# Kernel optimization log

Hardware: AMD Instinct MI355X
Metric: run time of the kernel (lower is better)

Reference implementation:

```python
import jax, jax.numpy as jnp
import numpy as np

TD_DENOM = 3600.0  # td_upper - td_lower
SD_DENOM = 1000.0  # sd_upper - sd_lower

B, T, E, H = 64, 256, 512, 512
V, NB = 50000, 128


def setup_inputs() -> dict:
    key = jax.random.key(0)
    ks = jax.random.split(key, 16)
    s = 0.02
    return {
        'loc_seq': jax.random.randint(ks[0], (B, T), 0, V),
        'td_upper_seq': jax.random.randint(ks[1], (B, T), 0, NB),
        'td_lower_seq': jax.random.randint(ks[2], (B, T), 0, NB),
        'sd_upper_seq': jax.random.randint(ks[3], (B, T), 0, NB),
        'sd_lower_seq': jax.random.randint(ks[4], (B, T), 0, NB),
        'valid_lengths': jax.random.randint(ks[5], (B,), 1, T + 1),
        'loc_emb': jax.random.normal(ks[6], (V, E), jnp.float32) * s,
        't_up_emb': jax.random.normal(ks[7], (NB, E), jnp.float32) * s,
        't_lo_emb': jax.random.normal(ks[8], (NB, E), jnp.float32) * s,
        's_up_emb': jax.random.normal(ks[9], (NB, E), jnp.float32) * s,
        's_lo_emb': jax.random.normal(ks[10], (NB, E), jnp.float32) * s,
        'Wt': jax.random.normal(ks[11], (E, 3 * H), jnp.float32) * s,
        'Ws': jax.random.normal(ks[12], (E, 3 * H), jnp.float32) * s,
        'Wi': jax.random.normal(ks[13], (E, 4 * H), jnp.float32) * s,
        'bi': jnp.zeros((4 * H,), jnp.float32),
        'Wh': jax.random.normal(ks[14], (H, 4 * H), jnp.float32) * s,
    }


def reference(loc_seq, td_upper_seq, td_lower_seq, sd_upper_seq, sd_lower_seq,
              valid_lengths, loc_emb, t_up_emb, t_lo_emb, s_up_emb, s_lo_emb,
              Wt, Ws, Wi, bi, Wh):
    Bs, Ts = loc_seq.shape
    Hs = Wh.shape[0]
    x = loc_emb[loc_seq]                                            # (B,T,E)
    q = (t_up_emb[td_upper_seq] + t_lo_emb[td_lower_seq]) / TD_DENOM
    sp = (s_up_emb[sd_upper_seq] + s_lo_emb[sd_lower_seq]) / SD_DENOM
    # first_step zeroes q and s
    mask = (jnp.arange(Ts) > 0).astype(x.dtype)[None, :, None]
    q = q * mask
    sp = sp * mask
    Fp = jnp.einsum('bte,ef->btf', q, Wt) + jnp.einsum('bte,ef->btf', sp, Ws)  # (B,T,3H)
    xp = jnp.einsum('bte,ef->btf', x, Wi) + bi                                  # (B,T,4H)

    def step(carry, xs):
        h, c = carry
        xpt, Ft = xs
        tmp = xpt + h @ Wh
        i_t, f_t, o_t, g_t = jnp.split(tmp, 4, axis=1)
        i_F, f_F, o_F = jnp.split(Ft, 3, axis=1)
        i_t = jax.nn.sigmoid(i_t + i_F)
        f_t = jax.nn.sigmoid(f_t + f_F)
        o_t = jax.nn.sigmoid(o_t + o_F)
        g_t = jnp.tanh(g_t)
        c = f_t * c + i_t * g_t
        h = o_t * jnp.tanh(c)
        return (h, c), (h, c)

    h0 = jnp.zeros((Bs, Hs), x.dtype)
    c0 = jnp.zeros((Bs, Hs), x.dtype)
    (hT, cT), (hs, cs) = jax.lax.scan(
        step, (h0, c0), (xp.transpose(1, 0, 2), Fp.transpose(1, 0, 2)))
    all_h = hs.transpose(1, 0, 2)  # (B,T,H)
    all_c = cs.transpose(1, 0, 2)
    # original prepends the final hidden, then selects index (valid_length+1)-1
    all_h_full = jnp.concatenate([hT[:, None], all_h], axis=1)  # (B,T+1,H)
    all_c_full = jnp.concatenate([cT[:, None], all_c], axis=1)
    b_idx = jnp.arange(Bs)
    last_h = all_h_full[b_idx, valid_lengths]
    last_c = all_c_full[b_idx, valid_lengths]
    return (all_h, last_h, last_c)
```

## Files before the change

### kernel.cpp

```cpp
#include <hip/hip_runtime.h>
#include <stdint.h>

#define A_CAT_OFF  0ull
#define WCT_OFF    50331648ull
#define WHR_OFF    56623104ull
#define G_OFF      58720256ull
#define HBUF_OFF   125829120ull
#define WS_NEED    126091264ull

typedef short bf16x8 __attribute__((ext_vector_type(8)));
typedef float f32x4  __attribute__((ext_vector_type(4)));

__device__ __forceinline__ unsigned short f2bf(float f) {
  union { float f; uint32_t u; } v; v.f = f;
  uint32_t u = v.u;
  u += 0x7FFFu + ((u >> 16) & 1u);
  return (unsigned short)(u >> 16);
}
__device__ __forceinline__ float bf2f(unsigned short h) {
  union { uint32_t u; float f; } v; v.u = ((uint32_t)h) << 16;
  return v.f;
}
__device__ __forceinline__ float u2f(uint32_t u) {
  union { uint32_t u; float f; } v; v.u = u; return v.f;
}
__device__ __forceinline__ uint32_t f2u(float f) {
  union { float f; uint32_t u; } v; v.f = f; return v.u;
}
__device__ __forceinline__ float fsigmoid(float x) { return 1.0f / (1.0f + __expf(-x)); }
__device__ __forceinline__ float ftanh(float x) {
  float e = __expf(2.0f * x);
  return 1.0f - 2.0f / (e + 1.0f);
}
__device__ __forceinline__ uint4 pack8(const unsigned short* v) {
  uint4 r;
  r.x = (uint32_t)v[0] | ((uint32_t)v[1] << 16);
  r.y = (uint32_t)v[2] | ((uint32_t)v[3] << 16);
  r.z = (uint32_t)v[4] | ((uint32_t)v[5] << 16);
  r.w = (uint32_t)v[6] | ((uint32_t)v[7] << 16);
  return r;
}

#define GLOAD_LDS16(GP, LP)                                                   \
  __builtin_amdgcn_global_load_lds(                                          \
      (const __attribute__((address_space(1))) uint32_t*)(GP),               \
      (__attribute__((address_space(3))) uint32_t*)(LP), 16, 0, 0)

__global__ __launch_bounds__(256) void k_prep(
    const float* __restrict__ Wi, const float* __restrict__ Wt,
    const float* __restrict__ Ws, const float* __restrict__ Wh,
    uint8_t* ws) {
  int id = blockIdx.x * 256 + threadIdx.x;
  if (id < 393216) {
    int n  = id & 2047;
    int k0 = (id >> 11) << 3;
    unsigned short v[8];
#pragma unroll
    for (int j = 0; j < 8; ++j) {
      int k = k0 + j;
      float x;
      if (k < 512)       x = Wi[k * 2048 + n];
      else if (k < 1024) x = (n < 1536) ? Wt[(k - 512) * 1536 + n] : 0.0f;
      else               x = (n < 1536) ? Ws[(k - 1024) * 1536 + n] : 0.0f;
      v[j] = f2bf(x);
    }
    size_t off = WCT_OFF + (size_t)n * 3072 +
                 (size_t)(((uint32_t)k0 * 2u) ^ (((uint32_t)n & 7u) << 4));
    *(uint4*)(ws + off) = pack8(v);
  } else if (id < 524288) {
    int id2 = id - 393216;
    int cc  = id2 & 2047;
    int k0  = (id2 >> 11) << 3;
    int col = ((cc >> 5) & 3) * 512 + (cc >> 7) * 32 + (cc & 31);
    unsigned short v[8];
#pragma unroll
    for (int j = 0; j < 8; ++j) v[j] = f2bf(Wh[(size_t)(k0 + j) * 2048 + col]);
    size_t off = WHR_OFF + (size_t)cc * 1024 +
                 (size_t)(((uint32_t)k0 * 2u) ^ (((uint32_t)cc & 7u) << 4));
    *(uint4*)(ws + off) = pack8(v);
  } else if (id < 532480) {
    uint4 z; z.x = z.y = z.z = z.w = 0u;
    *(uint4*)(ws + HBUF_OFF + (size_t)(id - 524288) * 16) = z;
  } else {
    uint4 z; z.x = z.y = z.z = z.w = 1u;
    *(uint4*)(ws + HBUF_OFF + 131072ull + (size_t)(id - 532480) * 16) = z;
  }
}

__global__ __launch_bounds__(192) void k_gather(
    const int* __restrict__ loc, const int* __restrict__ tdu,
    const int* __restrict__ tdl, const int* __restrict__ sdu,
    const int* __restrict__ sdl,
    const float* __restrict__ loc_emb, const float* __restrict__ tup,
    const float* __restrict__ tlo, const float* __restrict__ sup,
    const float* __restrict__ slo, uint8_t* ws) {
  int m  = blockIdx.x;
  int t  = m & 255;
  int k0 = threadIdx.x << 3;
  float vals[8];
  if (k0 < 512) {
    const float* s = loc_emb + (size_t)loc[m] * 512 + k0;
#pragma unroll
    for (int j = 0; j < 8; ++j) vals[j] = s[j];
  } else if (k0 < 1024) {
    int e = k0 - 512;
    const float* a = tup + (size_t)tdu[m] * 512 + e;
    const float* b = tlo + (size_t)tdl[m] * 512 + e;
    float sc = (t > 0) ? (1.0f / 3600.0f) : 0.0f;
#pragma unroll
    for (int j = 0; j < 8; ++j) vals[j] = (a[j] + b[j]) * sc;
  } else {
    int e = k0 - 1024;
    const float* a = sup + (size_t)sdu[m] * 512 + e;
    const float* b = slo + (size_t)sdl[m] * 512 + e;
    float sc = (t > 0) ? (1.0f / 1000.0f) : 0.0f;
#pragma unroll
    for (int j = 0; j < 8; ++j) vals[j] = (a[j] + b[j]) * sc;
  }
  unsigned short v[8];
#pragma unroll
  for (int j = 0; j < 8; ++j) v[j] = f2bf(vals[j]);
  size_t off = A_CAT_OFF + (size_t)m * 3072 +
               (size_t)(((uint32_t)k0 * 2u) ^ (((uint32_t)m & 7u) << 4));
  *(uint4*)(ws + off) = pack8(v);
}

__global__ __launch_bounds__(256) void k_gemm(uint8_t* ws,
                                              const float* __restrict__ bi) {
  __shared__ uint8_t A_lds[16384];
  __shared__ uint8_t B_lds[16384];
  const uint8_t* Acat = ws + A_CAT_OFF;
  const uint8_t* Wct  = ws + WCT_OFF;
  uint8_t* Gp = ws + G_OFF;
  int tid = threadIdx.x;
  int lane = tid & 63, wave = tid >> 6;
  int wm = wave >> 1, wn = wave & 1;
  int tile_m = blockIdx.x >> 4, tile_n = blockIdx.x & 15;

  f32x4 acc[4][4];
#pragma unroll
  for (int m = 0; m < 4; ++m)
#pragma unroll
    for (int n = 0; n < 4; ++n) acc[m][n] = f32x4{0.f, 0.f, 0.f, 0.f};

  for (int kb = 0; kb < 1536; kb += 64) {
#pragma unroll
    for (int i = 0; i < 4; ++i) {
      int lidx = i * 256 + tid;
      int row = lidx >> 3, ch = lidx & 7;
      GLOAD_LDS16(Acat + (size_t)(tile_m * 128 + row) * 3072 + kb * 2 + ch * 16,
                  A_lds + (i * 256 + wave * 64) * 16);
    }
#pragma unroll
    for (int i = 0; i < 4; ++i) {
      int lidx = i * 256 + tid;
      int row = lidx >> 3, ch = lidx & 7;
      GLOAD_LDS16(Wct + (size_t)(tile_n * 128 + row) * 3072 + kb * 2 + ch * 16,
                  B_lds + (i * 256 + wave * 64) * 16);
    }
    __syncthreads();
#pragma unroll
    for (int kk = 0; kk < 2; ++kk) {
      int koff = kk * 64 + ((lane >> 4) << 4);
      bf16x8 af[4], bfr[4];
#pragma unroll
      for (int m = 0; m < 4; ++m) {
        int row = wm * 64 + m * 16 + (lane & 15);
        af[m] = *(const bf16x8*)(A_lds + row * 128 + (koff ^ ((row & 7) << 4)));
      }
#pragma unroll
      for (int n = 0; n < 4; ++n) {
        int row = wn * 64 + n * 16 + (lane & 15);
        bfr[n] = *(const bf16x8*)(B_lds + row * 128 + (koff ^ ((row & 7) << 4)));
      }
#pragma unroll
      for (int m = 0; m < 4; ++m)
#pragma unroll
        for (int n = 0; n < 4; ++n)
          acc[m][n] = __builtin_amdgcn_mfma_f32_16x16x32_bf16(af[m], bfr[n],
                                                              acc[m][n], 0, 0, 0);
    }
    __syncthreads();
  }
  int lr = lane >> 4, lc = lane & 15;
#pragma unroll
  for (int n = 0; n < 4; ++n) {
    int gcol = tile_n * 128 + wn * 64 + n * 16 + lc;
    float bv = bi[gcol];
#pragma unroll
    for (int m = 0; m < 4; ++m) {
      int growb = tile_m * 128 + wm * 64 + m * 16 + lr * 4;
#pragma unroll
      for (int q = 0; q < 4; ++q) {
        int grow = growb + q;
        float v = acc[m][n][q] + bv;
        size_t gi = ((size_t)(grow & 255) * 64 + (size_t)(grow >> 8)) * 2048 + gcol;
        *(unsigned short*)(Gp + gi * 2) = f2bf(v);
      }
    }
  }
}

__global__ __launch_bounds__(256) void k_recur(uint8_t* ws,
                                               const int* __restrict__ vlen,
                                               float* __restrict__ out) {
  extern __shared__ uint8_t smem[];
  uint8_t* Wh_lds = smem;
  uint8_t* h_lds  = smem + 131072;
  float*   tmp    = (float*)(smem + 147456);

  int tid = threadIdx.x, bid = blockIdx.x;
  int lane = tid & 63, wave = tid >> 6;
  int r = bid >> 4, c = bid & 15;

  const uint8_t* Gp  = ws + G_OFF;
  const uint8_t* Whr = ws + WHR_OFF;

  {
    const uint8_t* src = Whr + (size_t)c * 131072;
#pragma unroll
    for (int i = 0; i < 32; ++i) {
      int cb = i * 256 + wave * 64;
      GLOAD_LDS16(src + (size_t)(cb + lane) * 16, Wh_lds + (size_t)cb * 16);
    }
  }

  int gb_b = tid >> 4;
  int d0 = (tid & 15) << 1;
  int gbatch = r * 16 + gb_b;
  int vl = vlen[gbatch];
  float cr0 = 0.0f, cr1 = 0.0f;
  float* outH  = out;
  float* outLH = out + 8388608;
  float* outLC = out + 8421376;

  __syncthreads();

  for (int t = 0; t < 256; ++t) {
    uint32_t gv[4];
    {
      size_t gidx = ((size_t)(t * 64 + gbatch) * 2048 + (size_t)(c * 32 + d0));
#pragma unroll
      for (int g = 0; g < 4; ++g)
        gv[g] = *(const uint32_t*)(Gp + (gidx + (size_t)g * 512) * 2);
    }

    uint64_t x[16];
    {
      uint64_t* hb64 = (uint64_t*)(ws + HBUF_OFF + (size_t)(t & 1) * 131072 +
                                   (size_t)r * 32768);
      uint32_t expect = (uint32_t)((t >> 1) & 1);
      uint32_t okm = 0;
      while (okm != 0xFFFFu) {
#pragma unroll
        for (int i = 0; i < 16; ++i)
          if (!(okm & (1u << i)))
            x[i] = __hip_atomic_load(&hb64[i * 256 + tid], __ATOMIC_RELAXED,
                                     __HIP_MEMORY_SCOPE_AGENT);
#pragma unroll
        for (int i = 0; i < 16; ++i)
          if (!(okm & (1u << i))) {
            uint32_t lo = (uint32_t)x[i], hi = (uint32_t)(x[i] >> 32);
            if ((((lo ^ expect) & 1u) | ((hi ^ expect) & 1u)) == 0u)
              okm |= (1u << i);
          }
      }
    }
#pragma unroll
    for (int i = 0; i < 16; ++i) {
      uint32_t lo = (uint32_t)x[i], hi = (uint32_t)(x[i] >> 32);
      uint32_t pk = (uint32_t)f2bf(u2f(lo)) | ((uint32_t)f2bf(u2f(hi)) << 16);
      *(uint32_t*)(h_lds + i * 1024 + ((tid * 4) ^ ((i & 7) << 4))) = pk;
    }
    __syncthreads();

    f32x4 acc0 = f32x4{0.f, 0.f, 0.f, 0.f}, acc1 = acc0;
    {
      int lrow = lane & 15;
      int g16 = (lane >> 4) << 4;
      int rb0 = wave * 32 + lrow;
      int rb1 = rb0 + 16;
      int aswz = (lrow & 7) << 4;
      int bswz0 = (rb0 & 7) << 4;
      int bswz1 = (rb1 & 7) << 4;
#pragma unroll
      for (int kk = 0; kk < 16; ++kk) {
        int ko = kk * 64 + g16;
        bf16x8 a  = *(const bf16x8*)(h_lds + lrow * 1024 + (ko ^ aswz));
        bf16x8 b0 = *(const bf16x8*)(Wh_lds + (size_t)rb0 * 1024 + (ko ^ bswz0));
        bf16x8 b1 = *(const bf16x8*)(Wh_lds + (size_t)rb1 * 1024 + (ko ^ bswz1));
        acc0 = __builtin_amdgcn_mfma_f32_16x16x32_bf16(a, b0, acc0, 0, 0, 0);
        acc1 = __builtin_amdgcn_mfma_f32_16x16x32_bf16(a, b1, acc1, 0, 0, 0);
      }
    }
    {
      int colb = wave * 32 + (lane & 15);
      int rowd = (lane >> 4) << 2;
#pragma unroll
      for (int q = 0; q < 4; ++q) {
        tmp[(rowd + q) * 129 + colb]      = acc0[q];
        tmp[(rowd + q) * 129 + colb + 16] = acc1[q];
      }
    }
    __syncthreads();

    {
      float h2[2], c2[2];
      int tb = gb_b * 129 + d0;
#pragma unroll
      for (int u = 0; u < 2; ++u) {
        float ip = tmp[tb + u]      + bf2f((unsigned short)((gv[0] >> (16 * u)) & 0xFFFF));
        float fp = tmp[tb + u + 32] + bf2f((unsigned short)((gv[1] >> (16 * u)) & 0xFFFF));
        float op = tmp[tb + u + 64] + bf2f((unsigned short)((gv[2] >> (16 * u)) & 0xFFFF));
        float gp = tmp[tb + u + 96] + bf2f((unsigned short)((gv[3] >> (16 * u)) & 0xFFFF));
        float ig = fsigmoid(ip), fg = fsigmoid(fp), og = fsigmoid(op);
        float gt = ftanh(gp);
        float cold = u ? cr1 : cr0;
        float cnew = fg * cold + ig * gt;
        if (u) cr1 = cnew; else cr0 = cnew;
        h2[u] = og * ftanh(cnew);
        c2[u] = cnew;
      }
      {
        uint32_t wtag = (uint32_t)(((t + 1) >> 1) & 1);
        uint32_t w0 = (f2u(h2[0]) & ~1u) | wtag;
        uint32_t w1 = (f2u(h2[1]) & ~1u) | wtag;
        uint64_t pv = (uint64_t)w0 | ((uint64_t)w1 << 32);
        uint64_t* hw64 = (uint64_t*)(ws + HBUF_OFF + (size_t)((t + 1) & 1) * 131072);
        __hip_atomic_store(&hw64[((size_t)gbatch * 512 + (size_t)(c * 32 + d0)) >> 1],
                           pv, __ATOMIC_RELAXED, __HIP_MEMORY_SCOPE_AGENT);
      }
      size_t ob = ((size_t)gbatch * 256 + (size_t)t) * 512 + (size_t)(c * 32 + d0);
      float2 hv; hv.x = h2[0]; hv.y = h2[1];
      *(float2*)(outH + ob) = hv;
      if (t == vl - 1) {
        size_t lb = (size_t)gbatch * 512 + (size_t)(c * 32 + d0);
        float2 cv; cv.x = c2[0]; cv.y = c2[1];
        *(float2*)(outLH + lb) = hv;
        *(float2*)(outLC + lb) = cv;
      }
    }
  }
}

extern "C" void kernel_launch(void* const* d_in, const int* in_sizes, int n_in,
                              void* d_out, int out_size, void* d_ws, size_t ws_size,
                              hipStream_t stream) {
  const int*   loc     = (const int*)d_in[0];
  const int*   tdu     = (const int*)d_in[1];
  const int*   tdl     = (const int*)d_in[2];
  const int*   sdu     = (const int*)d_in[3];
  const int*   sdl     = (const int*)d_in[4];
  const int*   vlen    = (const int*)d_in[5];
  const float* loc_emb = (const float*)d_in[6];
  const float* tup     = (const float*)d_in[7];
  const float* tlo     = (const float*)d_in[8];
  const float* sup     = (const float*)d_in[9];
  const float* slo     = (const float*)d_in[10];
  const float* Wt      = (const float*)d_in[11];
  const float* Ws      = (const float*)d_in[12];
  const float* Wi      = (const float*)d_in[13];
  const float* bi      = (const float*)d_in[14];
  const float* Wh      = (const float*)d_in[15];
  uint8_t* ws = (uint8_t*)d_ws;
  float* out = (float*)d_out;

  if (ws_size < WS_NEED) return;

  (void)hipFuncSetAttribute((const void*)k_recur,
                            hipFuncAttributeMaxDynamicSharedMemorySize, 155712);

  k_prep  <<<2112, 256, 0, stream>>>(Wi, Wt, Ws, Wh, ws);
  k_gather<<<16384, 192, 0, stream>>>(loc, tdu, tdl, sdu, sdl,
                                      loc_emb, tup, tlo, sup, slo, ws);
  k_gemm  <<<2048, 256, 0, stream>>>(ws, bi);
  k_recur <<<64, 256, 155712, stream>>>(ws, vlen, out);
}
```

Before: 1.158 ms.

## Spread recurrence blocks across XCDs and streamline cross-block h polling

The recurrent kernel now launches 128 blocks and has half exit immediately, remapping (row group, column slice) so the working blocks are spread across chiplets in a chosen pattern. The polling loop uses non-temporal sc0 inline-asm loads with one waitcnt per pass, falling back to atomic loads after many passes. The h publish is now issued twice, a plain store followed by the atomic one. Gate preactivations are prefetched one step ahead, and the LDS transpose scratch uses pitch 130 so it can be read as float2. The intent is lower per-step cross-block sync latency, at the cost of relying on the assumed block-to-XCD placement and on cache-bypass semantics for correctness.

```diff
diff --git a/kernel.cpp b/kernel.cpp
--- a/kernel.cpp
+++ b/kernel.cpp
@@ -204,14 +204,17 @@
 __global__ __launch_bounds__(256) void k_recur(uint8_t* ws,
                                                const int* __restrict__ vlen,
                                                float* __restrict__ out) {
+  int bid = blockIdx.x;
+  if ((bid & 7) >= 4) return;
+  int r = bid & 7, c = bid >> 3;
+
   extern __shared__ uint8_t smem[];
   uint8_t* Wh_lds = smem;
   uint8_t* h_lds  = smem + 131072;
   float*   tmp    = (float*)(smem + 147456);
 
-  int tid = threadIdx.x, bid = blockIdx.x;
+  int tid = threadIdx.x;
   int lane = tid & 63, wave = tid >> 6;
-  int r = bid >> 4, c = bid & 15;
 
   const uint8_t* Gp  = ws + G_OFF;
   const uint8_t* Whr = ws + WHR_OFF;
@@ -230,40 +233,62 @@
   int gbatch = r * 16 + gb_b;
   int vl = vlen[gbatch];
   float cr0 = 0.0f, cr1 = 0.0f;
+  bool fb = false;
   float* outH  = out;
   float* outLH = out + 8388608;
   float* outLC = out + 8421376;
 
+  uint32_t gvc[4];
+  {
+    size_t gidx = ((size_t)gbatch * 2048 + (size_t)(c * 32 + d0));
+#pragma unroll
+    for (int g = 0; g < 4; ++g)
+      gvc[g] = *(const uint32_t*)(Gp + (gidx + (size_t)g * 512) * 2);
+  }
+
   __syncthreads();
 
   for (int t = 0; t < 256; ++t) {
-    uint32_t gv[4];
+    uint32_t gvn[4];
     {
-      size_t gidx = ((size_t)(t * 64 + gbatch) * 2048 + (size_t)(c * 32 + d0));
+      int tn = (t + 1) & 255;
+      size_t gidx = ((size_t)(tn * 64 + gbatch) * 2048 + (size_t)(c * 32 + d0));
 #pragma unroll
       for (int g = 0; g < 4; ++g)
-        gv[g] = *(const uint32_t*)(Gp + (gidx + (size_t)g * 512) * 2);
+        gvn[g] = *(const uint32_t*)(Gp + (gidx + (size_t)g * 512) * 2);
     }
 
     uint64_t x[16];
     {
-      uint64_t* hb64 = (uint64_t*)(ws + HBUF_OFF + (size_t)(t & 1) * 131072 +
-                                   (size_t)r * 32768);
+      const uint8_t* hb = ws + HBUF_OFF + (size_t)(t & 1) * 131072 +
+                          (size_t)r * 32768;
       uint32_t expect = (uint32_t)((t >> 1) & 1);
-      uint32_t okm = 0;
-      while (okm != 0xFFFFu) {
-#pragma unroll
-        for (int i = 0; i < 16; ++i)
-          if (!(okm & (1u << i)))
-            x[i] = __hip_atomic_load(&hb64[i * 256 + tid], __ATOMIC_RELAXED,
-                                     __HIP_MEMORY_SCOPE_AGENT);
-#pragma unroll
-        for (int i = 0; i < 16; ++i)
-          if (!(okm & (1u << i))) {
-            uint32_t lo = (uint32_t)x[i], hi = (uint32_t)(x[i] >> 32);
-            if ((((lo ^ expect) & 1u) | ((hi ^ expect) & 1u)) == 0u)
-              okm |= (1u << i);
+      int passes = 0;
+      for (;;) {
+        if (!fb) {
+#pragma unroll
+          for (int i = 0; i < 16; ++i) {
+            const void* p = hb + (size_t)i * 2048 + (size_t)tid * 8;
+            asm volatile("global_load_dwordx2 %0, %1, off sc0"
+                         : "=v"(x[i]) : "v"(p));
           }
+          asm volatile("s_waitcnt vmcnt(0)" ::: "memory");
+          __builtin_amdgcn_sched_barrier(0);
+        } else {
+#pragma unroll
+          for (int i = 0; i < 16; ++i)
+            x[i] = __hip_atomic_load(
+                (const uint64_t*)(hb + (size_t)i * 2048 + (size_t)tid * 8),
+                __ATOMIC_RELAXED, __HIP_MEMORY_SCOPE_AGENT);
+        }
+        uint32_t bad = 0;
+#pragma unroll
+        for (int i = 0; i < 16; ++i) {
+          uint32_t lo = (uint32_t)x[i], hi = (uint32_t)(x[i] >> 32);
+          bad |= ((lo ^ expect) & 1u) | ((hi ^ expect) & 1u);
+        }
+        if (!bad) break;
+        if (++passes > 64) fb = true;
       }
     }
 #pragma unroll
@@ -298,21 +323,25 @@
       int rowd = (lane >> 4) << 2;
 #pragma unroll
       for (int q = 0; q < 4; ++q) {
-        tmp[(rowd + q) * 129 + colb]      = acc0[q];
-        tmp[(rowd + q) * 129 + colb + 16] = acc1[q];
+        tmp[(rowd + q) * 130 + colb]      = acc0[q];
+        tmp[(rowd + q) * 130 + colb + 16] = acc1[q];
       }
     }
     __syncthreads();
 
     {
       float h2[2], c2[2];
-      int tb = gb_b * 129 + d0;
+      int tb = gb_b * 130 + d0;
+      float2 iP = *(float2*)&tmp[tb];
+      float2 fP = *(float2*)&tmp[tb + 32];
+      float2 oP = *(float2*)&tmp[tb + 64];
+      float2 gP = *(float2*)&tmp[tb + 96];
 #pragma unroll
       for (int u = 0; u < 2; ++u) {
-        float ip = tmp[tb + u]      + bf2f((unsigned short)((gv[0] >> (16 * u)) & 0xFFFF));
-        float fp = tmp[tb + u + 32] + bf2f((unsigned short)((gv[1] >> (16 * u)) & 0xFFFF));
-        float op = tmp[tb + u + 64] + bf2f((unsigned short)((gv[2] >> (16 * u)) & 0xFFFF));
-        float gp = tmp[tb + u + 96] + bf2f((unsigned short)((gv[3] >> (16 * u)) & 0xFFFF));
+        float ip = (u ? iP.y : iP.x) + bf2f((unsigned short)((gvc[0] >> (16 * u)) & 0xFFFF));
+        float fp = (u ? fP.y : fP.x) + bf2f((unsigned short)((gvc[1] >> (16 * u)) & 0xFFFF));
+        float op = (u ? oP.y : oP.x) + bf2f((unsigned short)((gvc[2] >> (16 * u)) & 0xFFFF));
+        float gp = (u ? gP.y : gP.x) + bf2f((unsigned short)((gvc[3] >> (16 * u)) & 0xFFFF));
         float ig = fsigmoid(ip), fg = fsigmoid(fp), og = fsigmoid(op);
         float gt = ftanh(gp);
         float cold = u ? cr1 : cr0;
@@ -327,8 +356,10 @@
         uint32_t w1 = (f2u(h2[1]) & ~1u) | wtag;
         uint64_t pv = (uint64_t)w0 | ((uint64_t)w1 << 32);
         uint64_t* hw64 = (uint64_t*)(ws + HBUF_OFF + (size_t)((t + 1) & 1) * 131072);
-        __hip_atomic_store(&hw64[((size_t)gbatch * 512 + (size_t)(c * 32 + d0)) >> 1],
-                           pv, __ATOMIC_RELAXED, __HIP_MEMORY_SCOPE_AGENT);
+        uint64_t* pub = &hw64[((size_t)gbatch * 512 + (size_t)(c * 32 + d0)) >> 1];
+        asm volatile("global_store_dwordx2 %0, %1, off"
+                     :: "v"(pub), "v"(pv) : "memory");
+        __hip_atomic_store(pub, pv, __ATOMIC_RELAXED, __HIP_MEMORY_SCOPE_AGENT);
       }
       size_t ob = ((size_t)gbatch * 256 + (size_t)t) * 512 + (size_t)(c * 32 + d0);
       float2 hv; hv.x = h2[0]; hv.y = h2[1];
@@ -340,6 +371,8 @@
         *(float2*)(outLC + lb) = cv;
       }
     }
+#pragma unroll
+    for (int g = 0; g < 4; ++g) gvc[g] = gvn[g];
   }
 }
 
@@ -368,11 +401,11 @@
   if (ws_size < WS_NEED) return;
 
   (void)hipFuncSetAttribute((const void*)k_recur,
-                            hipFuncAttributeMaxDynamicSharedMemorySize, 155712);
+                            hipFuncAttributeMaxDynamicSharedMemorySize, 155776);
 
   k_prep  <<<2112, 256, 0, stream>>>(Wi, Wt, Ws, Wh, ws);
   k_gather<<<16384, 192, 0, stream>>>(loc, tdu, tdl, sdu, sdl,
                                       loc_emb, tup, tlo, sup, slo, ws);
   k_gemm  <<<2048, 256, 0, stream>>>(ws, bi);
-  k_recur <<<64, 256, 155712, stream>>>(ws, vlen, out);
-}
+  k_recur <<<128, 256, 155776, stream>>>(ws, vlen, out);
+}
```

Result: slower. 1.223 ms (+5.6%).
